# Performance work log

Hardware: AMD Instinct MI355X
Metric: run time of the kernel (lower is better)

The kernel has to match this reference:

```python
import jax, jax.numpy as jnp
import numpy as np
import math

B, S, D = 2, 2048, 1024
H, KV, HD = 16, 4, 64
N_REP = H // KV
ROPE_THETA = 1.0e6


def _rope_tables(seq_len, head_dim, theta):
    inv_freq = 1.0 / (theta ** (np.arange(0, head_dim, 2, dtype=np.float32) / head_dim))
    t = np.arange(seq_len, dtype=np.float32)
    freqs = np.outer(t, inv_freq)                      # [S, HD/2]
    emb = np.concatenate([freqs, freqs], axis=-1)      # [S, HD]
    return jnp.asarray(np.cos(emb)), jnp.asarray(np.sin(emb))


def setup_inputs() -> dict:
    key = jax.random.key(0)
    ks = jax.random.split(key, 6)
    cos, sin = _rope_tables(S, HD, ROPE_THETA)
    scale = 0.02
    return {
        "x": jax.random.normal(ks[0], (B, S, D), dtype=jnp.float32),
        "cos": cos,
        "sin": sin,
        "Wq": jax.random.normal(ks[1], (D, H * HD), dtype=jnp.float32) * scale,
        "Wk": jax.random.normal(ks[2], (D, KV * HD), dtype=jnp.float32) * scale,
        "Wv": jax.random.normal(ks[3], (D, KV * HD), dtype=jnp.float32) * scale,
        "Wo": jax.random.normal(ks[4], (H * HD, D), dtype=jnp.float32) * scale,
    }


def _rotate_half(u):
    u1, u2 = u[..., : HD // 2], u[..., HD // 2 :]
    return jnp.concatenate([-u2, u1], axis=-1)


def reference(x, cos, sin, Wq, Wk, Wv, Wo):
    bsz, seq_len, _ = x.shape
    q = (x @ Wq).reshape(bsz, seq_len, H, HD)   # [B,S,H,HD]
    k = (x @ Wk).reshape(bsz, seq_len, KV, HD)  # [B,S,KV,HD]
    v = (x @ Wv).reshape(bsz, seq_len, KV, HD)

    # RoPE: cos/sin [S,HD] broadcast over batch and heads (unsqueeze_dim=1)
    c = cos[:seq_len][None, :, None, :]
    s = sin[:seq_len][None, :, None, :]
    q = q * c + _rotate_half(q) * s
    k = k * c + _rotate_half(k) * s

    # repeat_kv: expand KV heads groupwise to H heads
    k = jnp.repeat(k, N_REP, axis=2)  # [B,S,H,HD]
    v = jnp.repeat(v, N_REP, axis=2)

    q = q.transpose(0, 2, 1, 3)  # [B,H,S,HD]
    k = k.transpose(0, 2, 1, 3)
    v = v.transpose(0, 2, 1, 3)

    scores = jnp.einsum("bhqd,bhkd->bhqk", q, k) / math.sqrt(HD)
    causal = jnp.tril(jnp.ones((seq_len, seq_len), dtype=bool))
    scores = jnp.where(causal[None, None], scores, jnp.finfo(jnp.float32).min)
    probs = jax.nn.softmax(scores.astype(jnp.float32), axis=-1).astype(x.dtype)

    out = jnp.einsum("bhqk,bhkd->bhqd", probs, v)        # [B,H,S,HD]
    out = out.transpose(0, 2, 1, 3).reshape(bsz, seq_len, H * HD)
    return out @ Wo
```

## Files before the change

### kernel.cpp

```cpp
#include <hip/hip_runtime.h>

#define SS 2048
#define NH 16
#define NKV 4
#define HD 64

typedef __bf16 bf16;
typedef __bf16 bf16x8 __attribute__((ext_vector_type(8)));
typedef float f32x4 __attribute__((ext_vector_type(4)));

#define SM_SCALE 0.18033688011f

__device__ __forceinline__ void gl_lds16(const bf16* g, bf16* l) {
    __builtin_amdgcn_global_load_lds((const __attribute__((address_space(1))) void*)g,
                                     (__attribute__((address_space(3))) void*)l, 16, 0, 0);
}

__global__ __launch_bounds__(256) void prep_kernel(
    const float* __restrict__ x, const float* __restrict__ Wq, const float* __restrict__ Wk,
    const float* __restrict__ Wv, const float* __restrict__ Wo,
    bf16* __restrict__ xb, bf16* __restrict__ wqkv_t, bf16* __restrict__ wo_t)
{
    const int blk = blockIdx.x;
    const int tid = threadIdx.x;
    if (blk >= 640) {
        const float4* xv = (const float4*)x;
        const size_t base = (size_t)(blk - 640) * 2048 + tid;
        #pragma unroll
        for (int j = 0; j < 8; ++j) {
            const float4 v = xv[base + j * 256];
            bf16* o = xb + (base + j * 256) * 4;
            o[0] = (bf16)v.x; o[1] = (bf16)v.y; o[2] = (bf16)v.z; o[3] = (bf16)v.w;
        }
        return;
    }
    const float* W; bf16* Wt; int N, n0, k0;
    if (blk < 256)      { W = Wq; Wt = wqkv_t;                       N = 1024; n0 = (blk & 15) * 64;         k0 = (blk >> 4) * 64; }
    else if (blk < 320) { W = Wk; Wt = wqkv_t + (size_t)1024 * 1024; N = 256;  n0 = ((blk - 256) & 3) * 64;  k0 = ((blk - 256) >> 2) * 64; }
    else if (blk < 384) { W = Wv; Wt = wqkv_t + (size_t)1280 * 1024; N = 256;  n0 = ((blk - 320) & 3) * 64;  k0 = ((blk - 320) >> 2) * 64; }
    else                { W = Wo; Wt = wo_t;                         N = 1024; n0 = ((blk - 384) & 15) * 64; k0 = ((blk - 384) >> 4) * 64; }

    __shared__ float Ts[64][65];
    const int c = tid & 63, rr = tid >> 6;
    #pragma unroll
    for (int i = 0; i < 16; ++i) {
        const int kk = i * 4 + rr;
        Ts[kk][c] = W[(size_t)(k0 + kk) * N + n0 + c];
    }
    __syncthreads();
    #pragma unroll
    for (int i = 0; i < 16; ++i) {
        const int nn = i * 4 + rr;
        Wt[(size_t)(n0 + nn) * 1024 + k0 + c] = (bf16)Ts[c][nn];
    }
}

template<int EPI>
__global__ __launch_bounds__(512) void gemm_bt_kernel(
    const bf16* __restrict__ A, const bf16* __restrict__ Bt, float* __restrict__ C,
    const float* __restrict__ cosp, const float* __restrict__ sinp,
    bf16* __restrict__ qo, bf16* __restrict__ ko, bf16* __restrict__ vto,
    int M, int N, int K)
{
    __shared__ bf16 As[128 * 64];
    __shared__ bf16 Bs[128 * 64];
    const int m0 = blockIdx.x * 128, n0 = blockIdx.y * 128;
    const int tid = threadIdx.x;
    const int w = tid >> 6, lane = tid & 63, g = lane >> 4, li = lane & 15;
    const int wm = w >> 1, wn = w & 1;

    f32x4 acc[2][4];
    const f32x4 z = {0.f, 0.f, 0.f, 0.f};
    #pragma unroll
    for (int i = 0; i < 2; ++i)
        #pragma unroll
        for (int j = 0; j < 4; ++j) acc[i][j] = z;

    const int srow = tid >> 3;
    const int schunk = ((tid & 7) ^ (srow & 7)) * 8;
    const bf16* pA0 = A + (size_t)(m0 + srow) * K + schunk;
    const bf16* pA1 = A + (size_t)(m0 + 64 + srow) * K + schunk;
    const bf16* pB0 = Bt + (size_t)(n0 + srow) * K + schunk;
    const bf16* pB1 = Bt + (size_t)(n0 + 64 + srow) * K + schunk;
    bf16* lA0 = As + (size_t)w * 512;
    bf16* lA1 = As + 4096 + (size_t)w * 512;
    bf16* lB0 = Bs + (size_t)w * 512;
    bf16* lB1 = Bs + 4096 + (size_t)w * 512;

    for (int kk = 0; kk < K; kk += 64) {
        __syncthreads();
        gl_lds16(pA0 + kk, lA0);
        gl_lds16(pA1 + kk, lA1);
        gl_lds16(pB0 + kk, lB0);
        gl_lds16(pB1 + kk, lB1);
        __syncthreads();
        #pragma unroll
        for (int t = 0; t < 2; ++t) {
            bf16x8 af[2], bfr[4];
            #pragma unroll
            for (int mi = 0; mi < 2; ++mi) {
                const int row = wm * 32 + mi * 16 + li;
                af[mi] = *(const bf16x8*)&As[row * 64 + (((t * 4 + g) ^ (li & 7)) * 8)];
            }
            #pragma unroll
            for (int ni = 0; ni < 4; ++ni) {
                const int row = wn * 64 + ni * 16 + li;
                bfr[ni] = *(const bf16x8*)&Bs[row * 64 + (((t * 4 + g) ^ (li & 7)) * 8)];
            }
            #pragma unroll
            for (int mi = 0; mi < 2; ++mi)
                #pragma unroll
                for (int ni = 0; ni < 4; ++ni)
                    acc[mi][ni] = __builtin_amdgcn_mfma_f32_16x16x32_bf16(af[mi], bfr[ni], acc[mi][ni], 0, 0, 0);
        }
    }

    const int row0 = m0 + wm * 32, col0 = n0 + wn * 64;
    if (EPI == 0) {
        #pragma unroll
        for (int mi = 0; mi < 2; ++mi)
            #pragma unroll
            for (int ni = 0; ni < 4; ++ni)
                #pragma unroll
                for (int r = 0; r < 4; ++r)
                    C[(size_t)(row0 + mi * 16 + g * 4 + r) * N + col0 + ni * 16 + li] = acc[mi][ni][r];
    } else {
        #pragma unroll
        for (int ni = 0; ni < 4; ++ni) {
            const int col = col0 + ni * 16 + li;
            const int d = col & 63;
            #pragma unroll
            for (int mi = 0; mi < 2; ++mi) {
                #pragma unroll
                for (int r = 0; r < 4; ++r) {
                    const int row = row0 + mi * 16 + g * 4 + r;
                    const int bb = row >> 11, s = row & 2047;
                    float val = acc[mi][ni][r];
                    if (col < 1280) {
                        const float pairv = acc[mi][ni ^ 2][r];
                        const float rot = (d < 32) ? -pairv : pairv;
                        val = val * cosp[s * 64 + d] + rot * sinp[s * 64 + d];
                    }
                    if (col < 1024) {
                        const int hh = col >> 6;
                        qo[(((size_t)bb * NH + hh) * SS + s) * HD + d] = (bf16)(val * SM_SCALE);
                    } else if (col < 1280) {
                        const int kh = (col - 1024) >> 6;
                        ko[(((size_t)bb * NKV + kh) * SS + s) * HD + d] = (bf16)val;
                    } else {
                        const int kh = (col - 1280) >> 6;
                        vto[(((size_t)bb * NKV + kh) * HD + d) * SS + s] = (bf16)val;
                    }
                }
            }
        }
    }
}

#define FP 72
#define FPV 136
__global__ __launch_bounds__(256) void flash_kernel(const bf16* __restrict__ q, const bf16* __restrict__ k,
                                                    const bf16* __restrict__ vt, bf16* __restrict__ o)
{
    __shared__ bf16 Ks[128][FP];
    __shared__ bf16 Vt[64][FPV];
    __shared__ bf16 Ps[4][16][FP];

    const int blk = blockIdx.x;
    const int p = blk & 15;
    const int h = (blk >> 4) & 15;
    const int b = blk >> 8;
    const int kvh = h >> 2;
    const int tid = threadIdx.x;
    const int w = tid >> 6, lane = tid & 63, g = lane >> 4, li = lane & 15;

    const bf16* qh = q + ((size_t)b * NH + h) * SS * HD;
    const bf16* kh = k + ((size_t)b * NKV + kvh) * SS * HD;
    const bf16* vh = vt + ((size_t)b * NKV + kvh) * (size_t)HD * SS;

    bf16x8 ones;
    #pragma unroll
    for (int j = 0; j < 8; ++j) ones[j] = (bf16)1.0f;
    const f32x4 z = {0.f, 0.f, 0.f, 0.f};

    #pragma unroll
    for (int phase = 0; phase < 2; ++phase) {
        const int qt = phase ? p : (31 - p);

        const bf16* qrow = qh + (size_t)(qt * 64 + w * 16 + li) * HD;
        bf16x8 qf[2];
        qf[0] = *(const bf16x8*)(qrow + g * 8);
        qf[1] = *(const bf16x8*)(qrow + 32 + g * 8);

        f32x4 o_acc[4], l_acc;
        #pragma unroll
        for (int nt = 0; nt < 4; ++nt) o_acc[nt] = z;
        l_acc = z;

        for (int kt0 = 0; kt0 <= qt; kt0 += 2) {
            __syncthreads();
            {
                const int krow = tid >> 1, kcol = (tid & 1) * 32;
                const uint4* ks = (const uint4*)(kh + (size_t)(kt0 * 64 + krow) * HD + kcol);
                const uint4 a0 = ks[0], a1 = ks[1], a2 = ks[2], a3 = ks[3];
                *(uint4*)&Ks[krow][kcol]      = a0;
                *(uint4*)&Ks[krow][kcol + 8]  = a1;
                *(uint4*)&Ks[krow][kcol + 16] = a2;
                *(uint4*)&Ks[krow][kcol + 24] = a3;
                const int vrow = tid >> 2, vcol = (tid & 3) * 32;
                const uint4* vs = (const uint4*)(vh + (size_t)vrow * SS + kt0 * 64 + vcol);
                const uint4 c0 = vs[0], c1 = vs[1], c2 = vs[2], c3 = vs[3];
                *(uint4*)&Vt[vrow][vcol]      = c0;
                *(uint4*)&Vt[vrow][vcol + 8]  = c1;
                *(uint4*)&Vt[vrow][vcol + 16] = c2;
                *(uint4*)&Vt[vrow][vcol + 24] = c3;
            }
            __syncthreads();

            #pragma unroll
            for (int sub = 0; sub < 2; ++sub) {
                const int kt = kt0 + sub;
                if (kt > qt) break;

                f32x4 s_acc[4];
                #pragma unroll
                for (int nt = 0; nt < 4; ++nt) s_acc[nt] = z;
                #pragma unroll
                for (int t = 0; t < 2; ++t)
                    #pragma unroll
                    for (int nt = 0; nt < 4; ++nt) {
                        const bf16x8 kf = *(const bf16x8*)&Ks[sub * 64 + nt * 16 + li][t * 32 + g * 8];
                        s_acc[nt] = __builtin_amdgcn_mfma_f32_16x16x32_bf16(qf[t], kf, s_acc[nt], 0, 0, 0);
                    }

                if (kt == qt) {
                    const int qr0 = qt * 64 + w * 16 + g * 4;
                    #pragma unroll
                    for (int nt = 0; nt < 4; ++nt) {
                        const int key = kt * 64 + nt * 16 + li;
                        #pragma unroll
                        for (int r = 0; r < 4; ++r) {
                            float sv = s_acc[nt][r];
                            if (key > qr0 + r) sv = -1e30f;
                            Ps[w][g * 4 + r][(nt * 16 + li) ^ (g * 16)] = (bf16)exp2f(sv);
                        }
                    }
                } else {
                    #pragma unroll
                    for (int nt = 0; nt < 4; ++nt)
                        #pragma unroll
                        for (int r = 0; r < 4; ++r)
                            Ps[w][g * 4 + r][(nt * 16 + li) ^ (g * 16)] = (bf16)exp2f(s_acc[nt][r]);
                }

                #pragma unroll
                for (int t = 0; t < 2; ++t) {
                    const bf16x8 pf = *(const bf16x8*)&Ps[w][li][(t * 32 + g * 8) ^ ((li >> 2) * 16)];
                    l_acc = __builtin_amdgcn_mfma_f32_16x16x32_bf16(pf, ones, l_acc, 0, 0, 0);
                    #pragma unroll
                    for (int nt = 0; nt < 4; ++nt) {
                        const bf16x8 vf = *(const bf16x8*)&Vt[nt * 16 + li][sub * 64 + t * 32 + g * 8];
                        o_acc[nt] = __builtin_amdgcn_mfma_f32_16x16x32_bf16(pf, vf, o_acc[nt], 0, 0, 0);
                    }
                }
            }
        }

        #pragma unroll
        for (int r = 0; r < 4; ++r) {
            const float inv = 1.f / l_acc[r];
            const int s = qt * 64 + w * 16 + g * 4 + r;
            bf16* orow = o + (((size_t)b * SS + s) * NH + h) * HD;
            #pragma unroll
            for (int nt = 0; nt < 4; ++nt) orow[nt * 16 + li] = (bf16)(o_acc[nt][r] * inv);
        }
    }
}

extern "C" void kernel_launch(void* const* d_in, const int* in_sizes, int n_in,
                              void* d_out, int out_size, void* d_ws, size_t ws_size,
                              hipStream_t stream) {
    const float* x     = (const float*)d_in[0];
    const float* cos_t = (const float*)d_in[1];
    const float* sin_t = (const float*)d_in[2];
    const float* Wq    = (const float*)d_in[3];
    const float* Wk    = (const float*)d_in[4];
    const float* Wv    = (const float*)d_in[5];
    const float* Wo    = (const float*)d_in[6];
    float* out = (float*)d_out;

    char* wsb = (char*)d_ws;
    bf16* x_b    = (bf16*)(wsb);
    bf16* wqkv_t = (bf16*)(wsb + 8388608);
    bf16* wo_t   = (bf16*)(wsb + 11534336);
    bf16* q_b    = (bf16*)(wsb + 13631488);
    bf16* k_b    = (bf16*)(wsb + 22020096);
    bf16* vt_b   = (bf16*)(wsb + 24117248);
    bf16* o_b    = x_b;

    prep_kernel<<<1152, 256, 0, stream>>>(x, Wq, Wk, Wv, Wo, x_b, wqkv_t, wo_t);

    gemm_bt_kernel<2><<<dim3(32, 12), 512, 0, stream>>>(x_b, wqkv_t, nullptr, cos_t, sin_t,
                                                        q_b, k_b, vt_b, 4096, 1536, 1024);
    flash_kernel<<<512, 256, 0, stream>>>(q_b, k_b, vt_b, o_b);
    gemm_bt_kernel<0><<<dim3(32, 8), 512, 0, stream>>>(o_b, wo_t, out, nullptr, nullptr,
                                                       nullptr, nullptr, nullptr, 4096, 1024, 1024);
}
```

Baseline: 179.6 us.

## Shrink GEMM tiles to 128x64 and read flash K/V directly from global memory

```diff
diff --git a/kernel.cpp b/kernel.cpp
--- a/kernel.cpp
+++ b/kernel.cpp
@@ -56,18 +56,17 @@
 }
 
 template<int EPI>
-__global__ __launch_bounds__(512) void gemm_bt_kernel(
+__global__ __launch_bounds__(256) void gemm_bt_kernel(
     const bf16* __restrict__ A, const bf16* __restrict__ Bt, float* __restrict__ C,
     const float* __restrict__ cosp, const float* __restrict__ sinp,
     bf16* __restrict__ qo, bf16* __restrict__ ko, bf16* __restrict__ vto,
     int M, int N, int K)
 {
     __shared__ bf16 As[128 * 64];
-    __shared__ bf16 Bs[128 * 64];
-    const int m0 = blockIdx.x * 128, n0 = blockIdx.y * 128;
+    __shared__ bf16 Bs[64 * 64];
+    const int m0 = blockIdx.x * 128, n0 = blockIdx.y * 64;
     const int tid = threadIdx.x;
     const int w = tid >> 6, lane = tid & 63, g = lane >> 4, li = lane & 15;
-    const int wm = w >> 1, wn = w & 1;
 
     f32x4 acc[2][4];
     const f32x4 z = {0.f, 0.f, 0.f, 0.f};
@@ -79,34 +78,35 @@
     const int srow = tid >> 3;
     const int schunk = ((tid & 7) ^ (srow & 7)) * 8;
     const bf16* pA0 = A + (size_t)(m0 + srow) * K + schunk;
-    const bf16* pA1 = A + (size_t)(m0 + 64 + srow) * K + schunk;
+    const bf16* pA1 = A + (size_t)(m0 + 32 + srow) * K + schunk;
+    const bf16* pA2 = A + (size_t)(m0 + 64 + srow) * K + schunk;
+    const bf16* pA3 = A + (size_t)(m0 + 96 + srow) * K + schunk;
     const bf16* pB0 = Bt + (size_t)(n0 + srow) * K + schunk;
-    const bf16* pB1 = Bt + (size_t)(n0 + 64 + srow) * K + schunk;
+    const bf16* pB1 = Bt + (size_t)(n0 + 32 + srow) * K + schunk;
     bf16* lA0 = As + (size_t)w * 512;
-    bf16* lA1 = As + 4096 + (size_t)w * 512;
+    bf16* lA1 = As + 2048 + (size_t)w * 512;
+    bf16* lA2 = As + 4096 + (size_t)w * 512;
+    bf16* lA3 = As + 6144 + (size_t)w * 512;
     bf16* lB0 = Bs + (size_t)w * 512;
-    bf16* lB1 = Bs + 4096 + (size_t)w * 512;
+    bf16* lB1 = Bs + 2048 + (size_t)w * 512;
 
     for (int kk = 0; kk < K; kk += 64) {
         __syncthreads();
         gl_lds16(pA0 + kk, lA0);
         gl_lds16(pA1 + kk, lA1);
+        gl_lds16(pA2 + kk, lA2);
+        gl_lds16(pA3 + kk, lA3);
         gl_lds16(pB0 + kk, lB0);
         gl_lds16(pB1 + kk, lB1);
         __syncthreads();
         #pragma unroll
         for (int t = 0; t < 2; ++t) {
+            const int phys = ((t * 4 + g) ^ (li & 7)) * 8;
             bf16x8 af[2], bfr[4];
             #pragma unroll
-            for (int mi = 0; mi < 2; ++mi) {
-                const int row = wm * 32 + mi * 16 + li;
-                af[mi] = *(const bf16x8*)&As[row * 64 + (((t * 4 + g) ^ (li & 7)) * 8)];
-            }
-            #pragma unroll
-            for (int ni = 0; ni < 4; ++ni) {
-                const int row = wn * 64 + ni * 16 + li;
-                bfr[ni] = *(const bf16x8*)&Bs[row * 64 + (((t * 4 + g) ^ (li & 7)) * 8)];
-            }
+            for (int mi = 0; mi < 2; ++mi) af[mi] = *(const bf16x8*)&As[(w * 32 + mi * 16 + li) * 64 + phys];
+            #pragma unroll
+            for (int ni = 0; ni < 4; ++ni) bfr[ni] = *(const bf16x8*)&Bs[(ni * 16 + li) * 64 + phys];
             #pragma unroll
             for (int mi = 0; mi < 2; ++mi)
                 #pragma unroll
@@ -115,7 +115,7 @@
         }
     }
 
-    const int row0 = m0 + wm * 32, col0 = n0 + wn * 64;
+    const int row0 = m0 + w * 32;
     if (EPI == 0) {
         #pragma unroll
         for (int mi = 0; mi < 2; ++mi)
@@ -123,11 +123,11 @@
             for (int ni = 0; ni < 4; ++ni)
                 #pragma unroll
                 for (int r = 0; r < 4; ++r)
-                    C[(size_t)(row0 + mi * 16 + g * 4 + r) * N + col0 + ni * 16 + li] = acc[mi][ni][r];
+                    C[(size_t)(row0 + mi * 16 + g * 4 + r) * N + n0 + ni * 16 + li] = acc[mi][ni][r];
     } else {
         #pragma unroll
         for (int ni = 0; ni < 4; ++ni) {
-            const int col = col0 + ni * 16 + li;
+            const int col = n0 + ni * 16 + li;
             const int d = col & 63;
             #pragma unroll
             for (int mi = 0; mi < 2; ++mi) {
@@ -158,13 +158,10 @@
 }
 
 #define FP 72
-#define FPV 136
-__global__ __launch_bounds__(256) void flash_kernel(const bf16* __restrict__ q, const bf16* __restrict__ k,
+__global__ __launch_bounds__(512) void flash_kernel(const bf16* __restrict__ q, const bf16* __restrict__ k,
                                                     const bf16* __restrict__ vt, bf16* __restrict__ o)
 {
-    __shared__ bf16 Ks[128][FP];
-    __shared__ bf16 Vt[64][FPV];
-    __shared__ bf16 Ps[4][16][FP];
+    __shared__ bf16 Ps[8][16][FP];
 
     const int blk = blockIdx.x;
     const int p = blk & 15;
@@ -173,6 +170,8 @@
     const int kvh = h >> 2;
     const int tid = threadIdx.x;
     const int w = tid >> 6, lane = tid & 63, g = lane >> 4, li = lane & 15;
+    const int wg = w & 3;
+    const int qt = (w < 4) ? (31 - p) : p;
 
     const bf16* qh = q + ((size_t)b * NH + h) * SS * HD;
     const bf16* kh = k + ((size_t)b * NKV + kvh) * SS * HD;
@@ -183,97 +182,67 @@
     for (int j = 0; j < 8; ++j) ones[j] = (bf16)1.0f;
     const f32x4 z = {0.f, 0.f, 0.f, 0.f};
 
-    #pragma unroll
-    for (int phase = 0; phase < 2; ++phase) {
-        const int qt = phase ? p : (31 - p);
-
-        const bf16* qrow = qh + (size_t)(qt * 64 + w * 16 + li) * HD;
-        bf16x8 qf[2];
-        qf[0] = *(const bf16x8*)(qrow + g * 8);
-        qf[1] = *(const bf16x8*)(qrow + 32 + g * 8);
-
-        f32x4 o_acc[4], l_acc;
-        #pragma unroll
-        for (int nt = 0; nt < 4; ++nt) o_acc[nt] = z;
-        l_acc = z;
-
-        for (int kt0 = 0; kt0 <= qt; kt0 += 2) {
-            __syncthreads();
-            {
-                const int krow = tid >> 1, kcol = (tid & 1) * 32;
-                const uint4* ks = (const uint4*)(kh + (size_t)(kt0 * 64 + krow) * HD + kcol);
-                const uint4 a0 = ks[0], a1 = ks[1], a2 = ks[2], a3 = ks[3];
-                *(uint4*)&Ks[krow][kcol]      = a0;
-                *(uint4*)&Ks[krow][kcol + 8]  = a1;
-                *(uint4*)&Ks[krow][kcol + 16] = a2;
-                *(uint4*)&Ks[krow][kcol + 24] = a3;
-                const int vrow = tid >> 2, vcol = (tid & 3) * 32;
-                const uint4* vs = (const uint4*)(vh + (size_t)vrow * SS + kt0 * 64 + vcol);
-                const uint4 c0 = vs[0], c1 = vs[1], c2 = vs[2], c3 = vs[3];
-                *(uint4*)&Vt[vrow][vcol]      = c0;
-                *(uint4*)&Vt[vrow][vcol + 8]  = c1;
-                *(uint4*)&Vt[vrow][vcol + 16] = c2;
-                *(uint4*)&Vt[vrow][vcol + 24] = c3;
-            }
-            __syncthreads();
-
-            #pragma unroll
-            for (int sub = 0; sub < 2; ++sub) {
-                const int kt = kt0 + sub;
-                if (kt > qt) break;
-
-                f32x4 s_acc[4];
-                #pragma unroll
-                for (int nt = 0; nt < 4; ++nt) s_acc[nt] = z;
-                #pragma unroll
-                for (int t = 0; t < 2; ++t)
-                    #pragma unroll
-                    for (int nt = 0; nt < 4; ++nt) {
-                        const bf16x8 kf = *(const bf16x8*)&Ks[sub * 64 + nt * 16 + li][t * 32 + g * 8];
-                        s_acc[nt] = __builtin_amdgcn_mfma_f32_16x16x32_bf16(qf[t], kf, s_acc[nt], 0, 0, 0);
-                    }
-
-                if (kt == qt) {
-                    const int qr0 = qt * 64 + w * 16 + g * 4;
-                    #pragma unroll
-                    for (int nt = 0; nt < 4; ++nt) {
-                        const int key = kt * 64 + nt * 16 + li;
-                        #pragma unroll
-                        for (int r = 0; r < 4; ++r) {
-                            float sv = s_acc[nt][r];
-                            if (key > qr0 + r) sv = -1e30f;
-                            Ps[w][g * 4 + r][(nt * 16 + li) ^ (g * 16)] = (bf16)exp2f(sv);
-                        }
-                    }
-                } else {
-                    #pragma unroll
-                    for (int nt = 0; nt < 4; ++nt)
-                        #pragma unroll
-                        for (int r = 0; r < 4; ++r)
-                            Ps[w][g * 4 + r][(nt * 16 + li) ^ (g * 16)] = (bf16)exp2f(s_acc[nt][r]);
+    const bf16* qrow = qh + (size_t)(qt * 64 + wg * 16 + li) * HD;
+    bf16x8 qf[2];
+    qf[0] = *(const bf16x8*)(qrow + g * 8);
+    qf[1] = *(const bf16x8*)(qrow + 32 + g * 8);
+
+    f32x4 o_acc[4], l_acc;
+    #pragma unroll
+    for (int nt = 0; nt < 4; ++nt) o_acc[nt] = z;
+    l_acc = z;
+
+    for (int kt = 0; kt <= qt; ++kt) {
+        f32x4 s_acc[4];
+        #pragma unroll
+        for (int nt = 0; nt < 4; ++nt) s_acc[nt] = z;
+        #pragma unroll
+        for (int t = 0; t < 2; ++t)
+            #pragma unroll
+            for (int nt = 0; nt < 4; ++nt) {
+                const bf16x8 kf = *(const bf16x8*)(kh + (size_t)(kt * 64 + nt * 16 + li) * HD + t * 32 + g * 8);
+                s_acc[nt] = __builtin_amdgcn_mfma_f32_16x16x32_bf16(qf[t], kf, s_acc[nt], 0, 0, 0);
+            }
+
+        if (kt == qt) {
+            const int qr0 = qt * 64 + wg * 16 + g * 4;
+            #pragma unroll
+            for (int nt = 0; nt < 4; ++nt) {
+                const int key = kt * 64 + nt * 16 + li;
+                #pragma unroll
+                for (int r = 0; r < 4; ++r) {
+                    float sv = s_acc[nt][r];
+                    if (key > qr0 + r) sv = -1e30f;
+                    Ps[w][g * 4 + r][(nt * 16 + li) ^ (g * 16)] = (bf16)exp2f(sv);
                 }
-
-                #pragma unroll
-                for (int t = 0; t < 2; ++t) {
-                    const bf16x8 pf = *(const bf16x8*)&Ps[w][li][(t * 32 + g * 8) ^ ((li >> 2) * 16)];
-                    l_acc = __builtin_amdgcn_mfma_f32_16x16x32_bf16(pf, ones, l_acc, 0, 0, 0);
-                    #pragma unroll
-                    for (int nt = 0; nt < 4; ++nt) {
-                        const bf16x8 vf = *(const bf16x8*)&Vt[nt * 16 + li][sub * 64 + t * 32 + g * 8];
-                        o_acc[nt] = __builtin_amdgcn_mfma_f32_16x16x32_bf16(pf, vf, o_acc[nt], 0, 0, 0);
-                    }
-                }
-            }
-        }
-
-        #pragma unroll
-        for (int r = 0; r < 4; ++r) {
-            const float inv = 1.f / l_acc[r];
-            const int s = qt * 64 + w * 16 + g * 4 + r;
-            bf16* orow = o + (((size_t)b * SS + s) * NH + h) * HD;
-            #pragma unroll
-            for (int nt = 0; nt < 4; ++nt) orow[nt * 16 + li] = (bf16)(o_acc[nt][r] * inv);
-        }
+            }
+        } else {
+            #pragma unroll
+            for (int nt = 0; nt < 4; ++nt)
+                #pragma unroll
+                for (int r = 0; r < 4; ++r)
+                    Ps[w][g * 4 + r][(nt * 16 + li) ^ (g * 16)] = (bf16)exp2f(s_acc[nt][r]);
+        }
+
+        #pragma unroll
+        for (int t = 0; t < 2; ++t) {
+            const bf16x8 pf = *(const bf16x8*)&Ps[w][li][(t * 32 + g * 8) ^ ((li >> 2) * 16)];
+            l_acc = __builtin_amdgcn_mfma_f32_16x16x32_bf16(pf, ones, l_acc, 0, 0, 0);
+            #pragma unroll
+            for (int nt = 0; nt < 4; ++nt) {
+                const bf16x8 vf = *(const bf16x8*)(vh + (size_t)(nt * 16 + li) * SS + kt * 64 + t * 32 + g * 8);
+                o_acc[nt] = __builtin_amdgcn_mfma_f32_16x16x32_bf16(pf, vf, o_acc[nt], 0, 0, 0);
+            }
+        }
+    }
+
+    #pragma unroll
+    for (int r = 0; r < 4; ++r) {
+        const float inv = 1.f / l_acc[r];
+        const int s = qt * 64 + wg * 16 + g * 4 + r;
+        bf16* orow = o + (((size_t)b * SS + s) * NH + h) * HD;
+        #pragma unroll
+        for (int nt = 0; nt < 4; ++nt) orow[nt * 16 + li] = (bf16)(o_acc[nt][r] * inv);
     }
 }
 
@@ -300,9 +269,9 @@
 
     prep_kernel<<<1152, 256, 0, stream>>>(x, Wq, Wk, Wv, Wo, x_b, wqkv_t, wo_t);
 
-    gemm_bt_kernel<2><<<dim3(32, 12), 512, 0, stream>>>(x_b, wqkv_t, nullptr, cos_t, sin_t,
+    gemm_bt_kernel<2><<<dim3(32, 24), 256, 0, stream>>>(x_b, wqkv_t, nullptr, cos_t, sin_t,
                                                         q_b, k_b, vt_b, 4096, 1536, 1024);
-    flash_kernel<<<512, 256, 0, stream>>>(q_b, k_b, vt_b, o_b);
-    gemm_bt_kernel<0><<<dim3(32, 8), 512, 0, stream>>>(o_b, wo_t, out, nullptr, nullptr,
-                                                       nullptr, nullptr, nullptr, 4096, 1024, 1024);
-}
+    flash_kernel<<<512, 512, 0, stream>>>(q_b, k_b, vt_b, o_b);
+    gemm_bt_kernel<0><<<dim3(32, 16), 256, 0, stream>>>(o_b, wo_t, out, nullptr, nullptr,
+                                                        nullptr, nullptr, nullptr, 4096, 1024, 1024);
+}
```

Result: slower. 245.1 us (+36.5%).
